# Kernel tuning notes

Hardware: AMD Instinct MI355X
Metric: run time of the kernel (lower is better)

Reference implementation:

```python
import jax, jax.numpy as jnp
import numpy as np


def setup_inputs() -> dict:
    key = jax.random.key(0)
    k1, k2 = jax.random.split(key)
    B, N, M, D = 8, 8192, 8192, 3
    x = jax.random.normal(k1, (B, N, D), dtype=jnp.float32)
    y = jax.random.normal(k2, (B, M, D), dtype=jnp.float32)
    return {"x": x, "y": y}


def reference(x, y):
    # dist[b, i, j] = |x_bi|^2 + |y_bj|^2 - 2 * <x_bi, y_bj>
    # (same math as the torch code's rx.transpose(2,1) + ry - 2*xy, but
    #  computed with row-norm vectors instead of full NxN / MxM bmms)
    xx = jnp.sum(x * x, axis=-1)                      # [B, N]
    yy = jnp.sum(y * y, axis=-1)                      # [B, M]
    xy = jnp.einsum('bnd,bmd->bnm', x, y)             # [B, N, M]
    dist = xx[:, :, None] + yy[:, None, :] - 2.0 * xy # [B, N, M]
    dist1 = jnp.min(dist, axis=1)  # min over x points -> per-y nearest  [B, M]
    dist2 = jnp.min(dist, axis=2)  # min over y points -> per-x nearest  [B, N]
    return jnp.mean(dist1) + jnp.mean(dist2)
```

## Files before the change

### kernel.cpp

```cpp
#include <hip/hip_runtime.h>


#define B_ 8
#define N_ 8192
#define PTS (B_ * N_)
#define TPB 512

typedef short bf16x8 __attribute__((ext_vector_type(8)));
typedef float f32x16 __attribute__((ext_vector_type(16)));

__device__ __forceinline__ unsigned b16(float f) {
  unsigned u = __float_as_uint(f);
  return (u + 0x7FFFu + ((u >> 16) & 1u)) >> 16;
}
__device__ __forceinline__ float bf(unsigned h) { return __uint_as_float(h << 16); }

__global__ __launch_bounds__(256) void chamfer_pre_k(
    const float* __restrict__ x, const float* __restrict__ y,
    uint4* __restrict__ afX, uint4* __restrict__ bfX,
    uint4* __restrict__ afY, uint4* __restrict__ bfY,
    float* __restrict__ out) {
  int p = blockIdx.x * 256 + threadIdx.x;
  if (p == 0) out[0] = 0.0f;
  const unsigned one = 0x3F80u;
  int tile = p >> 5, m = p & 31;
  int i0 = tile * 64 + m, i1 = tile * 64 + 32 + m;

#pragma unroll
  for (int s = 0; s < 2; ++s) {
    const float* src = s ? y : x;
    uint4* af = s ? afY : afX;
    uint4* bf_ = s ? bfY : bfX;
    float v0 = src[3 * p], v1 = src[3 * p + 1], v2 = src[3 * p + 2];
    float nv = fmaf(v0, v0, fmaf(v1, v1, v2 * v2));
    unsigned nh = b16(nv), nl = b16(nv - bf(nh));
    float a0 = -2.0f * v0, a1 = -2.0f * v1, a2 = -2.0f * v2;
    unsigned ah0 = b16(a0), ah1 = b16(a1), ah2 = b16(a2);
    unsigned al0 = b16(a0 - bf(ah0)), al1 = b16(a1 - bf(ah1)), al2 = b16(a2 - bf(ah2));
    af[i0] = make_uint4(ah0 | (ah1 << 16), ah2 | (ah0 << 16),
                        ah1 | (ah2 << 16), al0 | (al1 << 16));
    af[i1] = make_uint4(al2 | (nh << 16), nl | (one << 16), one, 0u);
    unsigned yh0 = b16(v0), yh1 = b16(v1), yh2 = b16(v2);
    unsigned yl0 = b16(v0 - bf(yh0)), yl1 = b16(v1 - bf(yh1)), yl2 = b16(v2 - bf(yh2));
    bf_[i0] = make_uint4(yh0 | (yh1 << 16), yh2 | (yl0 << 16),
                         yl1 | (yl2 << 16), yh0 | (yh1 << 16));
    bf_[i1] = make_uint4(yh2 | (one << 16), one | (nh << 16), nl, 0u);
  }
}

__global__ __launch_bounds__(TPB, 4) void chamfer_main_k(
    const uint4* __restrict__ afX, const uint4* __restrict__ bfX,
    const uint4* __restrict__ afY, const uint4* __restrict__ bfY,
    float* __restrict__ gpart) {
  __shared__ uint4 ldsFrag[2][32 * 64];

  int t = threadIdx.x, lane = t & 63, w = t >> 6;
  int b = blockIdx.x;
  int g = b >> 1;
  int hf = b & 1;
  int dir = g >> 7;
  int gg = g & 127;
  int batch = gg >> 4;
  int seg = gg & 15;
  const uint4* __restrict__ arow = dir ? afY : afX;
  const uint4* __restrict__ bcand = dir ? bfX : bfY;

  int tb = batch * 256 + seg * 16 + w * 2;
  bf16x8 A0 = __builtin_bit_cast(bf16x8, arow[tb * 64 + lane]);
  bf16x8 A1 = __builtin_bit_cast(bf16x8, arow[(tb + 1) * 64 + lane]);

  f32x16 z = {0.f,0.f,0.f,0.f,0.f,0.f,0.f,0.f,0.f,0.f,0.f,0.f,0.f,0.f,0.f,0.f};
  f32x16 rm0, rm1;
#pragma unroll
  for (int r = 0; r < 16; ++r) { rm0[r] = 1e30f; rm1[r] = 1e30f; }

  const uint4* __restrict__ cb = bcand + (batch * 256 + hf * 128) * 64;
  uint4 stg[4];
#pragma unroll
  for (int k = 0; k < 4; ++k) stg[k] = cb[t + k * TPB];
#pragma unroll
  for (int k = 0; k < 4; ++k) ldsFrag[0][t + k * TPB] = stg[k];
  __syncthreads();

  for (int ch = 0; ch < 4; ++ch) {
    const uint4* cur = ldsFrag[ch & 1];
    if (ch < 3) {
      const uint4* nxt = cb + (ch + 1) * 2048;
#pragma unroll
      for (int k = 0; k < 4; ++k) stg[k] = nxt[t + k * TPB];
    }

    uint4 b0 = cur[lane], b1 = cur[64 + lane];
    for (int i = 0; i < 16; ++i) {
      uint4 nb0, nb1;
      if (i < 15) { nb0 = cur[(2 * i + 2) * 64 + lane]; nb1 = cur[(2 * i + 3) * 64 + lane]; }
      bf16x8 Bt0 = __builtin_bit_cast(bf16x8, b0);
      bf16x8 Bt1 = __builtin_bit_cast(bf16x8, b1);
      f32x16 acc0 = __builtin_amdgcn_mfma_f32_32x32x16_bf16(A0, Bt0, z, 0, 0, 0);
      f32x16 acc1 = __builtin_amdgcn_mfma_f32_32x32x16_bf16(A0, Bt1, z, 0, 0, 0);
      f32x16 acc2 = __builtin_amdgcn_mfma_f32_32x32x16_bf16(A1, Bt0, z, 0, 0, 0);
      f32x16 acc3 = __builtin_amdgcn_mfma_f32_32x32x16_bf16(A1, Bt1, z, 0, 0, 0);
#pragma unroll
      for (int r = 0; r < 16; ++r) {
        rm0[r] = fminf(fminf(rm0[r], acc0[r]), acc1[r]);
        rm1[r] = fminf(fminf(rm1[r], acc2[r]), acc3[r]);
      }
      b0 = nb0; b1 = nb1;
    }

    __syncthreads();
    if (ch < 3) {
      uint4* nbuf = ldsFrag[(ch + 1) & 1];
#pragma unroll
      for (int k = 0; k < 4; ++k) nbuf[t + k * TPB] = stg[k];
      __syncthreads();
    }
  }

#pragma unroll
  for (int msk = 1; msk <= 16; msk <<= 1)
#pragma unroll
    for (int r = 0; r < 16; ++r) {
      rm0[r] = fminf(rm0[r], __shfl_xor(rm0[r], msk, 64));
      rm1[r] = fminf(rm1[r], __shfl_xor(rm1[r], msk, 64));
    }

  float* gp = gpart + b * 512;
  if ((lane & 31) == 0) {
    int h = lane >> 5;
#pragma unroll
    for (int r = 0; r < 16; ++r) {
      int rr = (r & 3) + 8 * (r >> 2) + 4 * h;
      gp[w * 64 + rr] = rm0[r];
      gp[w * 64 + 32 + rr] = rm1[r];
    }
  }
}

__global__ __launch_bounds__(256) void chamfer_final_k(
    const float* __restrict__ gpart, float* __restrict__ out) {
  int i = blockIdx.x * 256 + threadIdx.x;
  float s = 0.0f;
#pragma unroll
  for (int e = 0; e < 4; ++e) {
    int rowid = 4 * i + e;
    int g = rowid >> 9, r = rowid & 511;
    s += fminf(gpart[(2 * g) * 512 + r], gpart[(2 * g + 1) * 512 + r]);
  }
  for (int off = 32; off > 0; off >>= 1) s += __shfl_down(s, off, 64);
  __shared__ float red[4];
  int lane = threadIdx.x & 63, wv = threadIdx.x >> 6;
  if (lane == 0) red[wv] = s;
  __syncthreads();
  if (threadIdx.x == 0) {
    float tt = (red[0] + red[1]) + (red[2] + red[3]);
    atomicAdd(out, tt * (1.0f / (float)PTS));
  }
}

extern "C" void kernel_launch(void* const* d_in, const int* in_sizes, int n_in,
                              void* d_out, int out_size, void* d_ws, size_t ws_size,
                              hipStream_t stream) {
  const float* x = (const float*)d_in[0];
  const float* y = (const float*)d_in[1];
  float* out = (float*)d_out;
  uint4* afX = (uint4*)d_ws;
  uint4* bfX = afX + 2048 * 64;
  uint4* afY = bfX + 2048 * 64;
  uint4* bfY = afY + 2048 * 64;
  float* gpart = (float*)(bfY + 2048 * 64);

  hipMemsetAsync(out, 0, sizeof(float), stream);
  chamfer_pre_k<<<PTS / 256, 256, 0, stream>>>(x, y, afX, bfX, afY, bfY, out);
  chamfer_main_k<<<512, TPB, 0, stream>>>(afX, bfX, afY, bfY, gpart);
  chamfer_final_k<<<128, 256, 0, stream>>>(gpart, out);
}
```

Baseline: 110.0 us.

## Stream candidate tiles into LDS via direct global-to-LDS loads

Replaces the register-staged global→LDS double buffering with __builtin_amdgcn_global_load_lds, so candidate chunks go straight into the alternate LDS buffer and one barrier per chunk is dropped. It also simplifies the inner loop (no software prefetch of B fragments, unroll 2, reordered MFMAs) and removes the redundant hipMemsetAsync, since the pre kernel already zeroes the output. This relies on the LDS DMA being complete by the next __syncthreads without an explicit vmcnt wait, which is a correctness risk if the compiler does not insert one.

```diff
diff --git a/kernel.cpp b/kernel.cpp
--- a/kernel.cpp
+++ b/kernel.cpp
@@ -8,6 +8,8 @@
 
 typedef short bf16x8 __attribute__((ext_vector_type(8)));
 typedef float f32x16 __attribute__((ext_vector_type(16)));
+typedef __attribute__((address_space(1))) const unsigned char ga_t;
+typedef __attribute__((address_space(3))) unsigned char la_t;
 
 __device__ __forceinline__ unsigned b16(float f) {
   unsigned u = __float_as_uint(f);
@@ -75,46 +77,38 @@
   for (int r = 0; r < 16; ++r) { rm0[r] = 1e30f; rm1[r] = 1e30f; }
 
   const uint4* __restrict__ cb = bcand + (batch * 256 + hf * 128) * 64;
-  uint4 stg[4];
+
+  auto dma_chunk = [&](int ch, int buf) {
 #pragma unroll
-  for (int k = 0; k < 4; ++k) stg[k] = cb[t + k * TPB];
-#pragma unroll
-  for (int k = 0; k < 4; ++k) ldsFrag[0][t + k * TPB] = stg[k];
+    for (int k = 0; k < 4; ++k) {
+      const uint4* gsrc = cb + ch * 2048 + k * 512 + w * 64 + lane;
+      uint4* ldst = &ldsFrag[buf][k * 512 + w * 64];
+      __builtin_amdgcn_global_load_lds((ga_t*)gsrc, (la_t*)ldst, 16, 0, 0);
+    }
+  };
+
+  dma_chunk(0, 0);
   __syncthreads();
 
   for (int ch = 0; ch < 4; ++ch) {
     const uint4* cur = ldsFrag[ch & 1];
-    if (ch < 3) {
-      const uint4* nxt = cb + (ch + 1) * 2048;
-#pragma unroll
-      for (int k = 0; k < 4; ++k) stg[k] = nxt[t + k * TPB];
-    }
+    if (ch < 3) dma_chunk(ch + 1, (ch + 1) & 1);
 
-    uint4 b0 = cur[lane], b1 = cur[64 + lane];
+#pragma unroll 2
     for (int i = 0; i < 16; ++i) {
-      uint4 nb0, nb1;
-      if (i < 15) { nb0 = cur[(2 * i + 2) * 64 + lane]; nb1 = cur[(2 * i + 3) * 64 + lane]; }
-      bf16x8 Bt0 = __builtin_bit_cast(bf16x8, b0);
-      bf16x8 Bt1 = __builtin_bit_cast(bf16x8, b1);
-      f32x16 acc0 = __builtin_amdgcn_mfma_f32_32x32x16_bf16(A0, Bt0, z, 0, 0, 0);
-      f32x16 acc1 = __builtin_amdgcn_mfma_f32_32x32x16_bf16(A0, Bt1, z, 0, 0, 0);
-      f32x16 acc2 = __builtin_amdgcn_mfma_f32_32x32x16_bf16(A1, Bt0, z, 0, 0, 0);
-      f32x16 acc3 = __builtin_amdgcn_mfma_f32_32x32x16_bf16(A1, Bt1, z, 0, 0, 0);
+      bf16x8 B0 = __builtin_bit_cast(bf16x8, cur[(2 * i) * 64 + lane]);
+      bf16x8 B1 = __builtin_bit_cast(bf16x8, cur[(2 * i + 1) * 64 + lane]);
+      f32x16 acc0 = __builtin_amdgcn_mfma_f32_32x32x16_bf16(A0, B0, z, 0, 0, 0);
+      f32x16 acc1 = __builtin_amdgcn_mfma_f32_32x32x16_bf16(A1, B0, z, 0, 0, 0);
+      f32x16 acc2 = __builtin_amdgcn_mfma_f32_32x32x16_bf16(A0, B1, z, 0, 0, 0);
+      f32x16 acc3 = __builtin_amdgcn_mfma_f32_32x32x16_bf16(A1, B1, z, 0, 0, 0);
 #pragma unroll
       for (int r = 0; r < 16; ++r) {
-        rm0[r] = fminf(fminf(rm0[r], acc0[r]), acc1[r]);
-        rm1[r] = fminf(fminf(rm1[r], acc2[r]), acc3[r]);
+        rm0[r] = fminf(fminf(rm0[r], acc0[r]), acc2[r]);
+        rm1[r] = fminf(fminf(rm1[r], acc1[r]), acc3[r]);
       }
-      b0 = nb0; b1 = nb1;
     }
-
     __syncthreads();
-    if (ch < 3) {
-      uint4* nbuf = ldsFrag[(ch + 1) & 1];
-#pragma unroll
-      for (int k = 0; k < 4; ++k) nbuf[t + k * TPB] = stg[k];
-      __syncthreads();
-    }
   }
 
 #pragma unroll
@@ -170,7 +164,6 @@
   uint4* bfY = afY + 2048 * 64;
   float* gpart = (float*)(bfY + 2048 * 64);
 
-  hipMemsetAsync(out, 0, sizeof(float), stream);
   chamfer_pre_k<<<PTS / 256, 256, 0, stream>>>(x, y, afX, bfX, afY, bfY, out);
   chamfer_main_k<<<512, TPB, 0, stream>>>(afX, bfX, afY, bfY, gpart);
   chamfer_final_k<<<128, 256, 0, stream>>>(gpart, out);
```

Measured after the change: 101.2 us. 1.09x faster.
